# Performance work log

Measured on AMD Instinct MI355X. Metric: run time of the kernel, lower is better.

The kernel has to match this reference:

```python
import jax, jax.numpy as jnp
import numpy as np
import math

BATCH, SEQ, D_MODEL, HEADS = 2, 2048, 1024, 16
DK = D_MODEL // HEADS  # 64
THETA = 10000.0


def _init_linear(key, d_in, d_out):
    std = math.sqrt(2.0 / (d_in + d_out))
    return (jax.random.truncated_normal(key, -3.0, 3.0, (d_in, d_out), jnp.float32) * std)


def setup_inputs() -> dict:
    key = jax.random.key(0)
    kx, kq, kk, kv, ko = jax.random.split(key, 5)
    x = jax.random.normal(kx, (BATCH, SEQ, D_MODEL), jnp.float32)
    W_Q = _init_linear(kq, D_MODEL, D_MODEL)
    W_K = _init_linear(kk, D_MODEL, D_MODEL)
    W_V = _init_linear(kv, D_MODEL, D_MODEL)
    W_O = _init_linear(ko, D_MODEL, D_MODEL)
    token_positions = jnp.arange(SEQ, dtype=jnp.int64 if jax.config.jax_enable_x64 else jnp.int32)
    # RoPE tables: angle[i, k] = i / theta**(2k/d_k), shape [max_seq_len, d_k//2]
    pos = jnp.arange(SEQ, dtype=jnp.float32)[:, None]
    inv_freq = THETA ** (-2.0 * jnp.arange(DK // 2, dtype=jnp.float32) / DK)
    angles = pos * inv_freq
    return {
        "x": x,
        "token_positions": token_positions,
        "W_Q": W_Q,
        "W_K": W_K,
        "W_V": W_V,
        "W_O": W_O,
        "cos": jnp.cos(angles),
        "sin": jnp.sin(angles),
    }


def _apply_rope(t, cos_p, sin_p):
    # t: [B, H, S, DK]; cos_p/sin_p: [S, DK//2] (already gathered by position)
    t_even = t[..., 0::2]
    t_odd = t[..., 1::2]
    even_rot = cos_p * t_even - sin_p * t_odd
    odd_rot = sin_p * t_even + cos_p * t_odd
    # interleave back: [..., DK//2, 2] -> [..., DK]
    return jnp.stack([even_rot, odd_rot], axis=-1).reshape(t.shape)


def reference(x, token_positions, W_Q, W_K, W_V, W_O, cos, sin):
    B, S, D = x.shape
    H, dk = HEADS, D // HEADS
    # QKV projections, split into heads: [B, S, D] -> [B, H, S, dk]
    def proj(W):
        return jnp.einsum("bsd,de->bse", x, W).reshape(B, S, H, dk).transpose(0, 2, 1, 3)
    Q, K, V = proj(W_Q), proj(W_K), proj(W_V)
    cos_p = cos[token_positions]  # [S, dk//2]
    sin_p = sin[token_positions]
    Q = _apply_rope(Q, cos_p, sin_p)
    K = _apply_rope(K, cos_p, sin_p)
    scores = jnp.einsum("bhqd,bhkd->bhqk", Q, K) / jnp.sqrt(jnp.asarray(dk, x.dtype))
    causal = jnp.tril(jnp.ones((S, S), dtype=bool))
    scores = jnp.where(causal, scores, -jnp.inf)
    attn = jax.nn.softmax(scores, axis=-1)
    out = jnp.einsum("bhqk,bhkd->bhqd", attn, V)  # [B, H, S, dk]
    out = out.transpose(0, 2, 1, 3).reshape(B, S, D)
    return jnp.einsum("bsd,de->bse", out, W_O)
```

## Files before the change

kernel.cpp:

```cpp
#include <hip/hip_runtime.h>

typedef unsigned short u16;
typedef unsigned int   u32;
typedef __bf16  bf16x8 __attribute__((ext_vector_type(8)));
typedef float   f32x4  __attribute__((ext_vector_type(4)));
typedef u32     u32x4  __attribute__((ext_vector_type(4)));

#define SEQ    2048
#define HEADS  16
#define DM     1024
#define NBH    32
#define NBS    4096

__device__ __forceinline__ u16 f2b(float f) {
    u32 x;
    __builtin_memcpy(&x, &f, 4);
    return (u16)((x + 0x7fffu + ((x >> 16) & 1u)) >> 16);
}

__device__ __forceinline__ u32 pk2(float lo, float hi) {
    return (u32)f2b(lo) | ((u32)f2b(hi) << 16);
}

__device__ __forceinline__ u32 pkc(float lo, float hi) {
    __bf16 a = (__bf16)lo, b = (__bf16)hi;
    u16 x, y;
    __builtin_memcpy(&x, &a, 2);
    __builtin_memcpy(&y, &b, 2);
    return (u32)x | ((u32)y << 16);
}

__device__ __forceinline__ bf16x8 ld_bf8(const u16* p) {
    return *(const bf16x8*)p;
}
__device__ __forceinline__ bf16x8 ld_f32x8_cvt(const float* p) {
    f32x4 a = *(const f32x4*)p;
    f32x4 b = *(const f32x4*)(p + 4);
    bf16x8 r;
    r[0] = (__bf16)a[0]; r[1] = (__bf16)a[1]; r[2] = (__bf16)a[2]; r[3] = (__bf16)a[3];
    r[4] = (__bf16)b[0]; r[5] = (__bf16)b[1]; r[6] = (__bf16)b[2]; r[7] = (__bf16)b[3];
    return r;
}

__device__ __forceinline__ void gl_lds16(const u16* g, __bf16* l) {
    __builtin_amdgcn_global_load_lds(
        (__attribute__((address_space(1))) void*)g,
        (__attribute__((address_space(3))) void*)l,
        16, 0, 0);
}

__global__ __launch_bounds__(256) void transpose_wqkv(const float* __restrict__ Wq,
                                                      const float* __restrict__ Wk,
                                                      const float* __restrict__ Wv,
                                                      u16* __restrict__ WqkvT) {
    __shared__ u16 tile[64][65];
    const int z  = blockIdx.z;
    const float* src = (z == 0) ? Wq : (z == 1) ? Wk : Wv;
    const int k0 = blockIdx.x * 64, n0 = blockIdx.y * 64;
    const int tid = threadIdx.x;
    for (int i = 0; i < 16; ++i) {
        int e = i * 256 + tid;
        int r = e >> 6, c = e & 63;
        tile[r][c] = f2b(src[(size_t)(k0 + r) * DM + n0 + c]);
    }
    __syncthreads();
    u16* dst = WqkvT + (size_t)z * DM * DM;
    for (int i = 0; i < 16; ++i) {
        int e = i * 256 + tid;
        int r = e >> 6, c = e & 63;
        dst[(size_t)(n0 + r) * DM + k0 + c] = tile[c][r];
    }
}

__global__ __launch_bounds__(256) void transpose_wo(const float* __restrict__ Wo,
                                                    u16* __restrict__ WoT) {
    __shared__ u16 tile[64][65];
    const int k0 = blockIdx.x * 64, n0 = blockIdx.y * 64;
    const int tid = threadIdx.x;
    for (int i = 0; i < 16; ++i) {
        int e = i * 256 + tid;
        int r = e >> 6, c = e & 63;
        tile[r][c] = f2b(Wo[(size_t)(k0 + r) * DM + n0 + c]);
    }
    __syncthreads();
    for (int i = 0; i < 16; ++i) {
        int e = i * 256 + tid;
        int r = e >> 6, c = e & 63;
        WoT[(size_t)(n0 + r) * DM + k0 + c] = tile[c][r];
    }
}


__global__ __launch_bounds__(256) void gemm_qkv(const float* __restrict__ Af,
                                                const u16* __restrict__ Bt,
                                                u16* __restrict__ Qp,
                                                u16* __restrict__ Kp,
                                                u16* __restrict__ Vt) {
    __shared__ __attribute__((aligned(16))) __bf16 As[128 * 64];
    __shared__ __attribute__((aligned(16))) __bf16 Bs[128 * 64];
    const int tid  = threadIdx.x;
    const int wave = tid >> 6, lane = tid & 63;
    const int quad = lane >> 4, col = lane & 15;
    const int wm = wave >> 1, wn = wave & 1;
    const int m0 = blockIdx.x * 128, n0 = blockIdx.y * 128;
    const int srow = tid >> 3;
    const int sc8  = (tid & 7) * 8;
    const int aslot = (((tid & 7) ^ (srow & 7)) << 3);
    const int c7 = col & 7;

    f32x4 zero = {0.f, 0.f, 0.f, 0.f};
    f32x4 acc[4][4];
    for (int i = 0; i < 4; ++i)
        for (int j = 0; j < 4; ++j) acc[i][j] = zero;

    bf16x8 av[4];
#pragma unroll
    for (int p = 0; p < 4; ++p)
        av[p] = ld_f32x8_cvt(Af + (size_t)(m0 + p * 32 + srow) * DM + sc8);

    for (int k0 = 0; k0 < DM; k0 += 64) {
        __syncthreads();
#pragma unroll
        for (int p = 0; p < 4; ++p)
            gl_lds16(Bt + (size_t)(n0 + p * 32 + srow) * DM + k0 + aslot,
                     &Bs[p * 2048 + tid * 8]);
#pragma unroll
        for (int p = 0; p < 4; ++p)
            *(bf16x8*)&As[(p * 32 + srow) * 64 + aslot] = av[p];
        __syncthreads();
        int kn = k0 + 64; if (kn >= DM) kn = k0;
#pragma unroll
        for (int p = 0; p < 4; ++p)
            av[p] = ld_f32x8_cvt(Af + (size_t)(m0 + p * 32 + srow) * DM + kn + sc8);
#pragma unroll
        for (int ks = 0; ks < 2; ++ks) {
            const int rsl = ((((ks << 2) | quad) ^ c7) << 3);
            bf16x8 af[4], bfr[4];
#pragma unroll
            for (int mt = 0; mt < 4; ++mt)
                af[mt] = *(const bf16x8*)&As[(wm * 64 + mt * 16 + col) * 64 + rsl];
#pragma unroll
            for (int nt = 0; nt < 4; ++nt)
                bfr[nt] = *(const bf16x8*)&Bs[(wn * 64 + nt * 16 + col) * 64 + rsl];
#pragma unroll
            for (int mt = 0; mt < 4; ++mt)
#pragma unroll
                for (int nt = 0; nt < 4; ++nt)
                    acc[mt][nt] = __builtin_amdgcn_mfma_f32_16x16x32_bf16(
                        af[mt], bfr[nt], acc[mt][nt], 0, 0, 0);
        }
    }

    for (int mt = 0; mt < 4; ++mt)
        for (int nt = 0; nt < 4; ++nt) {
            int cc = n0 + wn * 64 + nt * 16 + col;
            int which = cc >> 10;
            int c1 = cc & 1023;
            int h = c1 >> 6, d = c1 & 63;
            for (int r = 0; r < 4; ++r) {
                int row = m0 + wm * 64 + mt * 16 + quad * 4 + r;
                int b = row >> 11, s = row & (SEQ - 1);
                u16 val = f2b(acc[mt][nt][r]);
                size_t bh = (size_t)(b * HEADS + h);
                if (which == 0)
                    Qp[(bh * SEQ + s) * 64 + d] = val;
                else if (which == 1)
                    Kp[(bh * SEQ + s) * 64 + d] = val;
                else
                    Vt[(bh * 64 + d) * SEQ + s] = val;
            }
        }
}

__global__ __launch_bounds__(256) void gemm_wo(const u16* __restrict__ A,
                                               const u16* __restrict__ Bt,
                                               float* __restrict__ C) {
    __shared__ __attribute__((aligned(16))) __bf16 As[128 * 64];
    __shared__ __attribute__((aligned(16))) __bf16 Bs[128 * 64];
    const int tid  = threadIdx.x;
    const int wave = tid >> 6, lane = tid & 63;
    const int quad = lane >> 4, col = lane & 15;
    const int wm = wave >> 1, wn = wave & 1;
    const int m0 = blockIdx.x * 128, n0 = blockIdx.y * 128;
    const int srow = tid >> 3;
    const int aslot = (((tid & 7) ^ (srow & 7)) << 3);
    const int c7 = col & 7;

    f32x4 zero = {0.f, 0.f, 0.f, 0.f};
    f32x4 acc[4][4];
    for (int i = 0; i < 4; ++i)
        for (int j = 0; j < 4; ++j) acc[i][j] = zero;

    for (int k0 = 0; k0 < DM; k0 += 64) {
        __syncthreads();
#pragma unroll
        for (int p = 0; p < 4; ++p)
            gl_lds16(A + (size_t)(m0 + p * 32 + srow) * DM + k0 + aslot,
                     &As[p * 2048 + tid * 8]);
#pragma unroll
        for (int p = 0; p < 4; ++p)
            gl_lds16(Bt + (size_t)(n0 + p * 32 + srow) * DM + k0 + aslot,
                     &Bs[p * 2048 + tid * 8]);
        __syncthreads();
#pragma unroll
        for (int ks = 0; ks < 2; ++ks) {
            const int rsl = ((((ks << 2) | quad) ^ c7) << 3);
            bf16x8 af[4], bfr[4];
#pragma unroll
            for (int mt = 0; mt < 4; ++mt)
                af[mt] = *(const bf16x8*)&As[(wm * 64 + mt * 16 + col) * 64 + rsl];
#pragma unroll
            for (int nt = 0; nt < 4; ++nt)
                bfr[nt] = *(const bf16x8*)&Bs[(wn * 64 + nt * 16 + col) * 64 + rsl];
#pragma unroll
            for (int mt = 0; mt < 4; ++mt)
#pragma unroll
                for (int nt = 0; nt < 4; ++nt)
                    acc[mt][nt] = __builtin_amdgcn_mfma_f32_16x16x32_bf16(
                        af[mt], bfr[nt], acc[mt][nt], 0, 0, 0);
        }
    }

    for (int mt = 0; mt < 4; ++mt)
        for (int nt = 0; nt < 4; ++nt)
            for (int r = 0; r < 4; ++r) {
                int row = m0 + wm * 64 + mt * 16 + quad * 4 + r;
                int cc  = n0 + wn * 64 + nt * 16 + col;
                C[(size_t)row * DM + cc] = acc[mt][nt][r];
            }
}

__global__ __launch_bounds__(256) void rope_qk(u16* __restrict__ Qp,
                                               u16* __restrict__ Kp,
                                               const float* __restrict__ cosT,
                                               const float* __restrict__ sinT) {
    int t = blockIdx.x * 256 + threadIdx.x;
    int g  = t & 7;
    int s  = (t >> 3) & (SEQ - 1);
    int hh = (t >> 14) & (HEADS - 1);
    int b  = t >> 18;

    f32x4 cv = *(const f32x4*)&cosT[s * 32 + g * 4];
    f32x4 sv = *(const f32x4*)&sinT[s * 32 + g * 4];

    size_t addr = (((size_t)(b * HEADS + hh)) * SEQ + s) * 64 + g * 8;
    u32x4 q4 = *(const u32x4*)(Qp + addr);
    u32x4 k4 = *(const u32x4*)(Kp + addr);
    u32x4 qo4, ko4;
#pragma unroll
    for (int j = 0; j < 4; ++j) {
        u32 q2 = q4[j], k2 = k4[j];
        u32 qe_b = (q2 & 0xffff) << 16, qo_b = q2 & 0xffff0000u;
        u32 ke_b = (k2 & 0xffff) << 16, ko_b = k2 & 0xffff0000u;
        float qe, qo, ke, ko;
        __builtin_memcpy(&qe, &qe_b, 4); __builtin_memcpy(&qo, &qo_b, 4);
        __builtin_memcpy(&ke, &ke_b, 4); __builtin_memcpy(&ko, &ko_b, 4);
        qo4[j] = (u32)f2b(0.125f * (cv[j] * qe - sv[j] * qo)) |
                 ((u32)f2b(0.125f * (sv[j] * qe + cv[j] * qo)) << 16);
        ko4[j] = (u32)f2b(cv[j] * ke - sv[j] * ko) |
                 ((u32)f2b(sv[j] * ke + cv[j] * ko) << 16);
    }
    *(u32x4*)(Qp + addr) = qo4;
    *(u32x4*)(Kp + addr) = ko4;
}

__global__ __launch_bounds__(256, 3) void flash_attn(const u16* __restrict__ Qp,
                                                     const u16* __restrict__ Kp,
                                                     const u16* __restrict__ Vt,
                                                     u16* __restrict__ O) {
    __shared__ float os[4][32][68];
    __shared__ float mM[4][32];
    __shared__ float mL[4][32];
    const int tid  = threadIdx.x;
    const int wave = tid >> 6, lane = tid & 63;
    const int quad = lane >> 4, col = lane & 15;
    const bool hi5 = lane >= 32;
    const bool hi4 = (lane & 16) != 0;
    const int bh = blockIdx.x;
    const int b = bh >> 4, h = bh & 15;
    const int qt = 63 - blockIdx.y;
    const int q0 = qt * 32;

    const u16* Qb = Qp + (size_t)bh * SEQ * 64;
    const u16* Kb = Kp + (size_t)bh * SEQ * 64;
    const u16* Vb = Vt + (size_t)bh * 64 * SEQ;

    bf16x8 bq00 = ld_bf8(Qb + (size_t)(q0 + col) * 64 + quad * 8);
    bf16x8 bq01 = ld_bf8(Qb + (size_t)(q0 + col) * 64 + 32 + quad * 8);
    bf16x8 bq10 = ld_bf8(Qb + (size_t)(q0 + 16 + col) * 64 + quad * 8);
    bf16x8 bq11 = ld_bf8(Qb + (size_t)(q0 + 16 + col) * 64 + 32 + quad * 8);

    f32x4 zero = {0.f, 0.f, 0.f, 0.f};
    f32x4 o0[4] = {zero, zero, zero, zero};
    f32x4 o1[4] = {zero, zero, zero, zero};
    float m0_ = -1e30f, m1_ = -1e30f;
    float lp0 = 0.f, lp1 = 0.f;

    const int nkt = qt + 1;
    int kt = wave;
    bf16x8 ck00, ck01, ck10, ck11;
    if (kt < nkt) {
        const int kb = kt << 5;
        ck00 = ld_bf8(Kb + (size_t)(kb + col) * 64 + quad * 8);
        ck01 = ld_bf8(Kb + (size_t)(kb + col) * 64 + 32 + quad * 8);
        ck10 = ld_bf8(Kb + (size_t)(kb + 16 + col) * 64 + quad * 8);
        ck11 = ld_bf8(Kb + (size_t)(kb + 16 + col) * 64 + 32 + quad * 8);
    }

    for (; kt < nkt; kt += 4) {
        const int kb = kt << 5;
        bf16x8 bv0 = ld_bf8(Vb + (size_t)(0 * 16 + col) * SEQ + kb + quad * 8);
        bf16x8 bv1 = ld_bf8(Vb + (size_t)(1 * 16 + col) * SEQ + kb + quad * 8);
        bf16x8 bv2 = ld_bf8(Vb + (size_t)(2 * 16 + col) * SEQ + kb + quad * 8);
        bf16x8 bv3 = ld_bf8(Vb + (size_t)(3 * 16 + col) * SEQ + kb + quad * 8);
        int kn = kt + 4; if (kn >= nkt) kn = kt;
        const int kb2 = kn << 5;
        bf16x8 nk00 = ld_bf8(Kb + (size_t)(kb2 + col) * 64 + quad * 8);
        bf16x8 nk01 = ld_bf8(Kb + (size_t)(kb2 + col) * 64 + 32 + quad * 8);
        bf16x8 nk10 = ld_bf8(Kb + (size_t)(kb2 + 16 + col) * 64 + quad * 8);
        bf16x8 nk11 = ld_bf8(Kb + (size_t)(kb2 + 16 + col) * 64 + 32 + quad * 8);

        f32x4 s00 = zero, s01 = zero, s10 = zero, s11 = zero;
        s00 = __builtin_amdgcn_mfma_f32_16x16x32_bf16(ck00, bq00, s00, 0, 0, 0);
        s10 = __builtin_amdgcn_mfma_f32_16x16x32_bf16(ck00, bq10, s10, 0, 0, 0);
        s00 = __builtin_amdgcn_mfma_f32_16x16x32_bf16(ck01, bq01, s00, 0, 0, 0);
        s10 = __builtin_amdgcn_mfma_f32_16x16x32_bf16(ck01, bq11, s10, 0, 0, 0);
        s01 = __builtin_amdgcn_mfma_f32_16x16x32_bf16(ck10, bq00, s01, 0, 0, 0);
        s11 = __builtin_amdgcn_mfma_f32_16x16x32_bf16(ck10, bq10, s11, 0, 0, 0);
        s01 = __builtin_amdgcn_mfma_f32_16x16x32_bf16(ck11, bq01, s01, 0, 0, 0);
        s11 = __builtin_amdgcn_mfma_f32_16x16x32_bf16(ck11, bq11, s11, 0, 0, 0);

        float v00[4], v01[4], v10[4], v11[4];
        float lm0 = -1e30f, lm1 = -1e30f;
        if (kt == qt) {
            for (int r = 0; r < 4; ++r) {
                int krel = quad * 4 + r;
                float a0 = (krel > col) ? -1e30f : s00[r];
                float b0 = -1e30f;
                float a1 = s10[r];
                float b1 = (krel > col) ? -1e30f : s11[r];
                v00[r] = a0; v01[r] = b0; v10[r] = a1; v11[r] = b1;
                lm0 = fmaxf(lm0, fmaxf(a0, b0));
                lm1 = fmaxf(lm1, fmaxf(a1, b1));
            }
        } else {
            for (int r = 0; r < 4; ++r) {
                v00[r] = s00[r]; v01[r] = s01[r];
                v10[r] = s10[r]; v11[r] = s11[r];
                lm0 = fmaxf(lm0, fmaxf(v00[r], v01[r]));
                lm1 = fmaxf(lm1, fmaxf(v10[r], v11[r]));
            }
        }

        float dd = fmaxf(lm0 - m0_, lm1 - m1_);
        if (__any(dd > 8.f)) {
            float lr0 = fmaxf(lm0, __shfl_xor(lm0, 16));
            lr0 = fmaxf(lr0, __shfl_xor(lr0, 32));
            float lr1 = fmaxf(lm1, __shfl_xor(lm1, 16));
            lr1 = fmaxf(lr1, __shfl_xor(lr1, 32));
            float mn0 = fmaxf(m0_, lr0), mn1 = fmaxf(m1_, lr1);
            float al0 = __expf(m0_ - mn0), al1 = __expf(m1_ - mn1);
            m0_ = mn0; m1_ = mn1;
            lp0 *= al0; lp1 *= al1;
            for (int r = 0; r < 4; ++r) {
                float ar0 = __shfl(al0, quad * 4 + r);
                float ar1 = __shfl(al1, quad * 4 + r);
                for (int nt = 0; nt < 4; ++nt) {
                    o0[nt][r] *= ar0;
                    o1[nt][r] *= ar1;
                }
            }
        }

        for (int r = 0; r < 4; ++r) {
            v00[r] = __expf(v00[r] - m0_);
            v01[r] = __expf(v01[r] - m0_);
            v10[r] = __expf(v10[r] - m1_);
            v11[r] = __expf(v11[r] - m1_);
            lp0 += v00[r] + v01[r];
            lp1 += v10[r] + v11[r];
        }

        u32 fwa0[4], fwa1[4];
        {
            u32 A0 = pkc(v00[0], v00[1]), A1 = pkc(v00[2], v00[3]);
            u32 B0 = pkc(v01[0], v01[1]), B1 = pkc(v01[2], v01[3]);
            u32 g0 = hi5 ? A0 : B0,  g1 = hi5 ? A1 : B1;
            u32 r0 = __shfl_xor(g0, 32), r1 = __shfl_xor(g1, 32);
            u32 P00 = hi5 ? r0 : A0,  P01 = hi5 ? r1 : A1;
            u32 P10 = hi5 ? B0 : r0,  P11 = hi5 ? B1 : r1;
            u32 h0 = hi4 ? P00 : P10, h1 = hi4 ? P01 : P11;
            u32 u0 = __shfl_xor(h0, 16), u1 = __shfl_xor(h1, 16);
            fwa0[0] = hi4 ? u0 : P00;  fwa0[1] = hi4 ? u1 : P01;
            fwa0[2] = hi4 ? P10 : u0;  fwa0[3] = hi4 ? P11 : u1;
        }
        {
            u32 A0 = pkc(v10[0], v10[1]), A1 = pkc(v10[2], v10[3]);
            u32 B0 = pkc(v11[0], v11[1]), B1 = pkc(v11[2], v11[3]);
            u32 g0 = hi5 ? A0 : B0,  g1 = hi5 ? A1 : B1;
            u32 r0 = __shfl_xor(g0, 32), r1 = __shfl_xor(g1, 32);
            u32 P00 = hi5 ? r0 : A0,  P01 = hi5 ? r1 : A1;
            u32 P10 = hi5 ? B0 : r0,  P11 = hi5 ? B1 : r1;
            u32 h0 = hi4 ? P00 : P10, h1 = hi4 ? P01 : P11;
            u32 u0 = __shfl_xor(h0, 16), u1 = __shfl_xor(h1, 16);
            fwa1[0] = hi4 ? u0 : P00;  fwa1[1] = hi4 ? u1 : P01;
            fwa1[2] = hi4 ? P10 : u0;  fwa1[3] = hi4 ? P11 : u1;
        }
        bf16x8 pf0, pf1;
        __builtin_memcpy(&pf0, fwa0, 16);
        __builtin_memcpy(&pf1, fwa1, 16);

        o0[0] = __builtin_amdgcn_mfma_f32_16x16x32_bf16(pf0, bv0, o0[0], 0, 0, 0);
        o1[0] = __builtin_amdgcn_mfma_f32_16x16x32_bf16(pf1, bv0, o1[0], 0, 0, 0);
        o0[1] = __builtin_amdgcn_mfma_f32_16x16x32_bf16(pf0, bv1, o0[1], 0, 0, 0);
        o1[1] = __builtin_amdgcn_mfma_f32_16x16x32_bf16(pf1, bv1, o1[1], 0, 0, 0);
        o0[2] = __builtin_amdgcn_mfma_f32_16x16x32_bf16(pf0, bv2, o0[2], 0, 0, 0);
        o1[2] = __builtin_amdgcn_mfma_f32_16x16x32_bf16(pf1, bv2, o1[2], 0, 0, 0);
        o0[3] = __builtin_amdgcn_mfma_f32_16x16x32_bf16(pf0, bv3, o0[3], 0, 0, 0);
        o1[3] = __builtin_amdgcn_mfma_f32_16x16x32_bf16(pf1, bv3, o1[3], 0, 0, 0);

        ck00 = nk00; ck01 = nk01; ck10 = nk10; ck11 = nk11;
    }

    float lt0 = lp0;
    lt0 += __shfl_xor(lt0, 16); lt0 += __shfl_xor(lt0, 32);
    float lt1 = lp1;
    lt1 += __shfl_xor(lt1, 16); lt1 += __shfl_xor(lt1, 32);
    if (quad == 0) {
        mM[wave][col] = m0_;      mL[wave][col] = lt0;
        mM[wave][16 + col] = m1_; mL[wave][16 + col] = lt1;
    }
    for (int nt = 0; nt < 4; ++nt)
        for (int r = 0; r < 4; ++r) {
            os[wave][quad * 4 + r][nt * 16 + col]      = o0[nt][r];
            os[wave][16 + quad * 4 + r][nt * 16 + col] = o1[nt][r];
        }
    __syncthreads();

    {
        const int q  = tid >> 3;
        const int d0 = (tid & 7) * 8;
        float M = fmaxf(fmaxf(mM[0][q], mM[1][q]), fmaxf(mM[2][q], mM[3][q]));
        float L = 0.f;
        f32x4 a0 = {0.f, 0.f, 0.f, 0.f}, a1 = {0.f, 0.f, 0.f, 0.f};
        for (int w = 0; w < 4; ++w) {
            float e = __expf(mM[w][q] - M);
            L += e * mL[w][q];
            f32x4 p0 = *(const f32x4*)&os[w][q][d0];
            f32x4 p1 = *(const f32x4*)&os[w][q][d0 + 4];
            for (int j = 0; j < 4; ++j) { a0[j] += e * p0[j]; a1[j] += e * p1[j]; }
        }
        float inv = 1.f / L;
        u32x4 val;
        val[0] = pk2(a0[0] * inv, a0[1] * inv);
        val[1] = pk2(a0[2] * inv, a0[3] * inv);
        val[2] = pk2(a1[0] * inv, a1[1] * inv);
        val[3] = pk2(a1[2] * inv, a1[3] * inv);
        *(u32x4*)&O[((size_t)b * SEQ + q0 + q) * DM + h * 64 + d0] = val;
    }
}

extern "C" void kernel_launch(void* const* d_in, const int* in_sizes, int n_in,
                              void* d_out, int out_size, void* d_ws, size_t ws_size,
                              hipStream_t stream) {
    const float* x    = (const float*)d_in[0];
    const float* Wq   = (const float*)d_in[2];
    const float* Wk   = (const float*)d_in[3];
    const float* Wv   = (const float*)d_in[4];
    const float* Wo   = (const float*)d_in[5];
    const float* cosT = (const float*)d_in[6];
    const float* sinT = (const float*)d_in[7];
    float* out = (float*)d_out;

    u16* ws    = (u16*)d_ws;
    u16* qp    = ws;
    u16* kp    = ws + 4194304;
    u16* vt    = ws + 8388608;
    u16* woT   = ws + 8388608;
    u16* wqkvT = ws + 12582912;
    u16* ao    = ws + 12582912;

    dim3 blk(256);
    transpose_wqkv<<<dim3(16, 16, 3), blk, 0, stream>>>(Wq, Wk, Wv, wqkvT);
    gemm_qkv<<<dim3(32, 24), blk, 0, stream>>>(x, wqkvT, qp, kp, vt);
    rope_qk<<<dim3(2048), blk, 0, stream>>>(qp, kp, cosT, sinT);
    flash_attn<<<dim3(NBH, 64), blk, 0, stream>>>(qp, kp, vt, ao);
    transpose_wo<<<dim3(16, 16), blk, 0, stream>>>(Wo, woT);
    gemm_wo<<<dim3(32, 8), blk, 0, stream>>>(ao, woT, out);
}
```

Baseline: 245.3 us.

## Pre-convert x to bf16, retile Wo GEMM, exp2 softmax, prefetch V

Adds a separate kernel that converts x to bf16 into the output buffer, so the QKV GEMM can load A through direct global-to-LDS loads instead of converting in registers. The Wo GEMM is retiled to 128x64 blocks, doubling the grid for better CU occupancy. Attention folds log2(e) into the Q scale and uses exp2, with the rescale threshold adjusted to match, and V fragments are prefetched one iteration ahead like K. Final packing uses hardware bf16 conversion. These trade an extra kernel launch and a pass over x for cheaper GEMM loads, plus more registers in attention.

```diff
diff --git a/kernel.cpp b/kernel.cpp
--- a/kernel.cpp
+++ b/kernel.cpp
@@ -12,14 +12,12 @@
 #define NBH    32
 #define NBS    4096
 
+#define LOG2E  1.4426950408889634f
+
 __device__ __forceinline__ u16 f2b(float f) {
     u32 x;
     __builtin_memcpy(&x, &f, 4);
     return (u16)((x + 0x7fffu + ((x >> 16) & 1u)) >> 16);
-}
-
-__device__ __forceinline__ u32 pk2(float lo, float hi) {
-    return (u32)f2b(lo) | ((u32)f2b(hi) << 16);
 }
 
 __device__ __forceinline__ u32 pkc(float lo, float hi) {
@@ -32,14 +30,6 @@
 
 __device__ __forceinline__ bf16x8 ld_bf8(const u16* p) {
     return *(const bf16x8*)p;
-}
-__device__ __forceinline__ bf16x8 ld_f32x8_cvt(const float* p) {
-    f32x4 a = *(const f32x4*)p;
-    f32x4 b = *(const f32x4*)(p + 4);
-    bf16x8 r;
-    r[0] = (__bf16)a[0]; r[1] = (__bf16)a[1]; r[2] = (__bf16)a[2]; r[3] = (__bf16)a[3];
-    r[4] = (__bf16)b[0]; r[5] = (__bf16)b[1]; r[6] = (__bf16)b[2]; r[7] = (__bf16)b[3];
-    return r;
 }
 
 __device__ __forceinline__ void gl_lds16(const u16* g, __bf16* l) {
@@ -90,8 +80,21 @@
     }
 }
 
-
-__global__ __launch_bounds__(256) void gemm_qkv(const float* __restrict__ Af,
+__global__ __launch_bounds__(256) void cvt_x(const float* __restrict__ x,
+                                             u16* __restrict__ xb) {
+    int t = blockIdx.x * 256 + threadIdx.x;
+    const float* p = x + (size_t)t * 8;
+    f32x4 a = *(const f32x4*)p;
+    f32x4 b = *(const f32x4*)(p + 4);
+    u32x4 v;
+    v[0] = pkc(a[0], a[1]);
+    v[1] = pkc(a[2], a[3]);
+    v[2] = pkc(b[0], b[1]);
+    v[3] = pkc(b[2], b[3]);
+    *(u32x4*)(xb + (size_t)t * 8) = v;
+}
+
+__global__ __launch_bounds__(256) void gemm_qkv(const u16* __restrict__ Ab,
                                                 const u16* __restrict__ Bt,
                                                 u16* __restrict__ Qp,
                                                 u16* __restrict__ Kp,
@@ -104,7 +107,6 @@
     const int wm = wave >> 1, wn = wave & 1;
     const int m0 = blockIdx.x * 128, n0 = blockIdx.y * 128;
     const int srow = tid >> 3;
-    const int sc8  = (tid & 7) * 8;
     const int aslot = (((tid & 7) ^ (srow & 7)) << 3);
     const int c7 = col & 7;
 
@@ -113,25 +115,17 @@
     for (int i = 0; i < 4; ++i)
         for (int j = 0; j < 4; ++j) acc[i][j] = zero;
 
-    bf16x8 av[4];
-#pragma unroll
-    for (int p = 0; p < 4; ++p)
-        av[p] = ld_f32x8_cvt(Af + (size_t)(m0 + p * 32 + srow) * DM + sc8);
-
     for (int k0 = 0; k0 < DM; k0 += 64) {
         __syncthreads();
+#pragma unroll
+        for (int p = 0; p < 4; ++p)
+            gl_lds16(Ab + (size_t)(m0 + p * 32 + srow) * DM + k0 + aslot,
+                     &As[p * 2048 + tid * 8]);
 #pragma unroll
         for (int p = 0; p < 4; ++p)
             gl_lds16(Bt + (size_t)(n0 + p * 32 + srow) * DM + k0 + aslot,
                      &Bs[p * 2048 + tid * 8]);
-#pragma unroll
-        for (int p = 0; p < 4; ++p)
-            *(bf16x8*)&As[(p * 32 + srow) * 64 + aslot] = av[p];
         __syncthreads();
-        int kn = k0 + 64; if (kn >= DM) kn = k0;
-#pragma unroll
-        for (int p = 0; p < 4; ++p)
-            av[p] = ld_f32x8_cvt(Af + (size_t)(m0 + p * 32 + srow) * DM + kn + sc8);
 #pragma unroll
         for (int ks = 0; ks < 2; ++ks) {
             const int rsl = ((((ks << 2) | quad) ^ c7) << 3);
@@ -176,19 +170,18 @@
                                                const u16* __restrict__ Bt,
                                                float* __restrict__ C) {
     __shared__ __attribute__((aligned(16))) __bf16 As[128 * 64];
-    __shared__ __attribute__((aligned(16))) __bf16 Bs[128 * 64];
+    __shared__ __attribute__((aligned(16))) __bf16 Bs[64 * 64];
     const int tid  = threadIdx.x;
     const int wave = tid >> 6, lane = tid & 63;
     const int quad = lane >> 4, col = lane & 15;
-    const int wm = wave >> 1, wn = wave & 1;
-    const int m0 = blockIdx.x * 128, n0 = blockIdx.y * 128;
+    const int m0 = blockIdx.x * 128, n0 = blockIdx.y * 64;
     const int srow = tid >> 3;
     const int aslot = (((tid & 7) ^ (srow & 7)) << 3);
     const int c7 = col & 7;
 
     f32x4 zero = {0.f, 0.f, 0.f, 0.f};
-    f32x4 acc[4][4];
-    for (int i = 0; i < 4; ++i)
+    f32x4 acc[2][4];
+    for (int i = 0; i < 2; ++i)
         for (int j = 0; j < 4; ++j) acc[i][j] = zero;
 
     for (int k0 = 0; k0 < DM; k0 += 64) {
@@ -198,22 +191,22 @@
             gl_lds16(A + (size_t)(m0 + p * 32 + srow) * DM + k0 + aslot,
                      &As[p * 2048 + tid * 8]);
 #pragma unroll
-        for (int p = 0; p < 4; ++p)
+        for (int p = 0; p < 2; ++p)
             gl_lds16(Bt + (size_t)(n0 + p * 32 + srow) * DM + k0 + aslot,
                      &Bs[p * 2048 + tid * 8]);
         __syncthreads();
 #pragma unroll
         for (int ks = 0; ks < 2; ++ks) {
             const int rsl = ((((ks << 2) | quad) ^ c7) << 3);
-            bf16x8 af[4], bfr[4];
-#pragma unroll
-            for (int mt = 0; mt < 4; ++mt)
-                af[mt] = *(const bf16x8*)&As[(wm * 64 + mt * 16 + col) * 64 + rsl];
+            bf16x8 af[2], bfr[4];
+#pragma unroll
+            for (int mt = 0; mt < 2; ++mt)
+                af[mt] = *(const bf16x8*)&As[(wave * 32 + mt * 16 + col) * 64 + rsl];
 #pragma unroll
             for (int nt = 0; nt < 4; ++nt)
-                bfr[nt] = *(const bf16x8*)&Bs[(wn * 64 + nt * 16 + col) * 64 + rsl];
-#pragma unroll
-            for (int mt = 0; mt < 4; ++mt)
+                bfr[nt] = *(const bf16x8*)&Bs[(nt * 16 + col) * 64 + rsl];
+#pragma unroll
+            for (int mt = 0; mt < 2; ++mt)
 #pragma unroll
                 for (int nt = 0; nt < 4; ++nt)
                     acc[mt][nt] = __builtin_amdgcn_mfma_f32_16x16x32_bf16(
@@ -221,11 +214,11 @@
         }
     }
 
-    for (int mt = 0; mt < 4; ++mt)
+    for (int mt = 0; mt < 2; ++mt)
         for (int nt = 0; nt < 4; ++nt)
             for (int r = 0; r < 4; ++r) {
-                int row = m0 + wm * 64 + mt * 16 + quad * 4 + r;
-                int cc  = n0 + wn * 64 + nt * 16 + col;
+                int row = m0 + wave * 32 + mt * 16 + quad * 4 + r;
+                int cc  = n0 + nt * 16 + col;
                 C[(size_t)row * DM + cc] = acc[mt][nt][r];
             }
 }
@@ -243,6 +236,7 @@
     f32x4 cv = *(const f32x4*)&cosT[s * 32 + g * 4];
     f32x4 sv = *(const f32x4*)&sinT[s * 32 + g * 4];
 
+    const float QS = 0.125f * LOG2E;
     size_t addr = (((size_t)(b * HEADS + hh)) * SEQ + s) * 64 + g * 8;
     u32x4 q4 = *(const u32x4*)(Qp + addr);
     u32x4 k4 = *(const u32x4*)(Kp + addr);
@@ -255,8 +249,8 @@
         float qe, qo, ke, ko;
         __builtin_memcpy(&qe, &qe_b, 4); __builtin_memcpy(&qo, &qo_b, 4);
         __builtin_memcpy(&ke, &ke_b, 4); __builtin_memcpy(&ko, &ko_b, 4);
-        qo4[j] = (u32)f2b(0.125f * (cv[j] * qe - sv[j] * qo)) |
-                 ((u32)f2b(0.125f * (sv[j] * qe + cv[j] * qo)) << 16);
+        qo4[j] = (u32)f2b(QS * (cv[j] * qe - sv[j] * qo)) |
+                 ((u32)f2b(QS * (sv[j] * qe + cv[j] * qo)) << 16);
         ko4[j] = (u32)f2b(cv[j] * ke - sv[j] * ko) |
                  ((u32)f2b(sv[j] * ke + cv[j] * ko) << 16);
     }
@@ -298,27 +292,31 @@
 
     const int nkt = qt + 1;
     int kt = wave;
-    bf16x8 ck00, ck01, ck10, ck11;
+    bf16x8 ck00, ck01, ck10, ck11, cv0, cv1, cv2, cv3;
     if (kt < nkt) {
         const int kb = kt << 5;
         ck00 = ld_bf8(Kb + (size_t)(kb + col) * 64 + quad * 8);
         ck01 = ld_bf8(Kb + (size_t)(kb + col) * 64 + 32 + quad * 8);
         ck10 = ld_bf8(Kb + (size_t)(kb + 16 + col) * 64 + quad * 8);
         ck11 = ld_bf8(Kb + (size_t)(kb + 16 + col) * 64 + 32 + quad * 8);
+        cv0  = ld_bf8(Vb + (size_t)(0 * 16 + col) * SEQ + kb + quad * 8);
+        cv1  = ld_bf8(Vb + (size_t)(1 * 16 + col) * SEQ + kb + quad * 8);
+        cv2  = ld_bf8(Vb + (size_t)(2 * 16 + col) * SEQ + kb + quad * 8);
+        cv3  = ld_bf8(Vb + (size_t)(3 * 16 + col) * SEQ + kb + quad * 8);
     }
 
     for (; kt < nkt; kt += 4) {
         const int kb = kt << 5;
-        bf16x8 bv0 = ld_bf8(Vb + (size_t)(0 * 16 + col) * SEQ + kb + quad * 8);
-        bf16x8 bv1 = ld_bf8(Vb + (size_t)(1 * 16 + col) * SEQ + kb + quad * 8);
-        bf16x8 bv2 = ld_bf8(Vb + (size_t)(2 * 16 + col) * SEQ + kb + quad * 8);
-        bf16x8 bv3 = ld_bf8(Vb + (size_t)(3 * 16 + col) * SEQ + kb + quad * 8);
         int kn = kt + 4; if (kn >= nkt) kn = kt;
         const int kb2 = kn << 5;
         bf16x8 nk00 = ld_bf8(Kb + (size_t)(kb2 + col) * 64 + quad * 8);
         bf16x8 nk01 = ld_bf8(Kb + (size_t)(kb2 + col) * 64 + 32 + quad * 8);
         bf16x8 nk10 = ld_bf8(Kb + (size_t)(kb2 + 16 + col) * 64 + quad * 8);
         bf16x8 nk11 = ld_bf8(Kb + (size_t)(kb2 + 16 + col) * 64 + 32 + quad * 8);
+        bf16x8 nv0  = ld_bf8(Vb + (size_t)(0 * 16 + col) * SEQ + kb2 + quad * 8);
+        bf16x8 nv1  = ld_bf8(Vb + (size_t)(1 * 16 + col) * SEQ + kb2 + quad * 8);
+        bf16x8 nv2  = ld_bf8(Vb + (size_t)(2 * 16 + col) * SEQ + kb2 + quad * 8);
+        bf16x8 nv3  = ld_bf8(Vb + (size_t)(3 * 16 + col) * SEQ + kb2 + quad * 8);
 
         f32x4 s00 = zero, s01 = zero, s10 = zero, s11 = zero;
         s00 = __builtin_amdgcn_mfma_f32_16x16x32_bf16(ck00, bq00, s00, 0, 0, 0);
@@ -353,13 +351,14 @@
         }
 
         float dd = fmaxf(lm0 - m0_, lm1 - m1_);
-        if (__any(dd > 8.f)) {
+        if (__any(dd > 11.54f)) {
             float lr0 = fmaxf(lm0, __shfl_xor(lm0, 16));
             lr0 = fmaxf(lr0, __shfl_xor(lr0, 32));
             float lr1 = fmaxf(lm1, __shfl_xor(lm1, 16));
             lr1 = fmaxf(lr1, __shfl_xor(lr1, 32));
             float mn0 = fmaxf(m0_, lr0), mn1 = fmaxf(m1_, lr1);
-            float al0 = __expf(m0_ - mn0), al1 = __expf(m1_ - mn1);
+            float al0 = __builtin_amdgcn_exp2f(m0_ - mn0);
+            float al1 = __builtin_amdgcn_exp2f(m1_ - mn1);
             m0_ = mn0; m1_ = mn1;
             lp0 *= al0; lp1 *= al1;
             for (int r = 0; r < 4; ++r) {
@@ -373,10 +372,10 @@
         }
 
         for (int r = 0; r < 4; ++r) {
-            v00[r] = __expf(v00[r] - m0_);
-            v01[r] = __expf(v01[r] - m0_);
-            v10[r] = __expf(v10[r] - m1_);
-            v11[r] = __expf(v11[r] - m1_);
+            v00[r] = __builtin_amdgcn_exp2f(v00[r] - m0_);
+            v01[r] = __builtin_amdgcn_exp2f(v01[r] - m0_);
+            v10[r] = __builtin_amdgcn_exp2f(v10[r] - m1_);
+            v11[r] = __builtin_amdgcn_exp2f(v11[r] - m1_);
             lp0 += v00[r] + v01[r];
             lp1 += v10[r] + v11[r];
         }
@@ -410,16 +409,17 @@
         __builtin_memcpy(&pf0, fwa0, 16);
         __builtin_memcpy(&pf1, fwa1, 16);
 
-        o0[0] = __builtin_amdgcn_mfma_f32_16x16x32_bf16(pf0, bv0, o0[0], 0, 0, 0);
-        o1[0] = __builtin_amdgcn_mfma_f32_16x16x32_bf16(pf1, bv0, o1[0], 0, 0, 0);
-        o0[1] = __builtin_amdgcn_mfma_f32_16x16x32_bf16(pf0, bv1, o0[1], 0, 0, 0);
-        o1[1] = __builtin_amdgcn_mfma_f32_16x16x32_bf16(pf1, bv1, o1[1], 0, 0, 0);
-        o0[2] = __builtin_amdgcn_mfma_f32_16x16x32_bf16(pf0, bv2, o0[2], 0, 0, 0);
-        o1[2] = __builtin_amdgcn_mfma_f32_16x16x32_bf16(pf1, bv2, o1[2], 0, 0, 0);
-        o0[3] = __builtin_amdgcn_mfma_f32_16x16x32_bf16(pf0, bv3, o0[3], 0, 0, 0);
-        o1[3] = __builtin_amdgcn_mfma_f32_16x16x32_bf16(pf1, bv3, o1[3], 0, 0, 0);
+        o0[0] = __builtin_amdgcn_mfma_f32_16x16x32_bf16(pf0, cv0, o0[0], 0, 0, 0);
+        o1[0] = __builtin_amdgcn_mfma_f32_16x16x32_bf16(pf1, cv0, o1[0], 0, 0, 0);
+        o0[1] = __builtin_amdgcn_mfma_f32_16x16x32_bf16(pf0, cv1, o0[1], 0, 0, 0);
+        o1[1] = __builtin_amdgcn_mfma_f32_16x16x32_bf16(pf1, cv1, o1[1], 0, 0, 0);
+        o0[2] = __builtin_amdgcn_mfma_f32_16x16x32_bf16(pf0, cv2, o0[2], 0, 0, 0);
+        o1[2] = __builtin_amdgcn_mfma_f32_16x16x32_bf16(pf1, cv2, o1[2], 0, 0, 0);
+        o0[3] = __builtin_amdgcn_mfma_f32_16x16x32_bf16(pf0, cv3, o0[3], 0, 0, 0);
+        o1[3] = __builtin_amdgcn_mfma_f32_16x16x32_bf16(pf1, cv3, o1[3], 0, 0, 0);
 
         ck00 = nk00; ck01 = nk01; ck10 = nk10; ck11 = nk11;
+        cv0 = nv0; cv1 = nv1; cv2 = nv2; cv3 = nv3;
     }
 
     float lt0 = lp0;
@@ -444,7 +444,7 @@
         float L = 0.f;
         f32x4 a0 = {0.f, 0.f, 0.f, 0.f}, a1 = {0.f, 0.f, 0.f, 0.f};
         for (int w = 0; w < 4; ++w) {
-            float e = __expf(mM[w][q] - M);
+            float e = __builtin_amdgcn_exp2f(mM[w][q] - M);
             L += e * mL[w][q];
             f32x4 p0 = *(const f32x4*)&os[w][q][d0];
             f32x4 p1 = *(const f32x4*)&os[w][q][d0 + 4];
@@ -452,10 +452,10 @@
         }
         float inv = 1.f / L;
         u32x4 val;
-        val[0] = pk2(a0[0] * inv, a0[1] * inv);
-        val[1] = pk2(a0[2] * inv, a0[3] * inv);
-        val[2] = pk2(a1[0] * inv, a1[1] * inv);
-        val[3] = pk2(a1[2] * inv, a1[3] * inv);
+        val[0] = pkc(a0[0] * inv, a0[1] * inv);
+        val[1] = pkc(a0[2] * inv, a0[3] * inv);
+        val[2] = pkc(a1[0] * inv, a1[1] * inv);
+        val[3] = pkc(a1[2] * inv, a1[3] * inv);
         *(u32x4*)&O[((size_t)b * SEQ + q0 + q) * DM + h * 64 + d0] = val;
     }
 }
@@ -479,12 +479,14 @@
     u16* woT   = ws + 8388608;
     u16* wqkvT = ws + 12582912;
     u16* ao    = ws + 12582912;
+    u16* xb    = (u16*)out;
 
     dim3 blk(256);
     transpose_wqkv<<<dim3(16, 16, 3), blk, 0, stream>>>(Wq, Wk, Wv, wqkvT);
-    gemm_qkv<<<dim3(32, 24), blk, 0, stream>>>(x, wqkvT, qp, kp, vt);
+    cvt_x<<<dim3(2048), blk, 0, stream>>>(x, xb);
+    gemm_qkv<<<dim3(32, 24), blk, 0, stream>>>(xb, wqkvT, qp, kp, vt);
     rope_qk<<<dim3(2048), blk, 0, stream>>>(qp, kp, cosT, sinT);
     flash_attn<<<dim3(NBH, 64), blk, 0, stream>>>(qp, kp, vt, ao);
     transpose_wo<<<dim3(16, 16), blk, 0, stream>>>(Wo, woT);
-    gemm_wo<<<dim3(32, 8), blk, 0, stream>>>(ao, woT, out);
-}
+    gemm_wo<<<dim3(32, 16), blk, 0, stream>>>(ao, woT, out);
+}
```

Measured after the change: 233.5 us. 1.05x faster.
